# Kernel tuning notes

Measured on AMD Instinct MI355X. Metric: run time of the kernel, lower is better.

Reference implementation:

```python
import jax, jax.numpy as jnp
import numpy as np

SELECT_NUM = 5
N_OBJ = 256


def conv(x, w, b, stride=1, pad=None):
    """NCHW conv. pad=None -> VALID; pad=1 -> [(1,1),(1,1)]."""
    padding = 'VALID' if pad is None else [(pad, pad), (pad, pad)]
    out = jax.lax.conv_general_dilated(
        x, w, (stride, stride), padding,
        dimension_numbers=('NCHW', 'OIHW', 'NCHW'))
    return out + b[None, :, None, None]


def setup_inputs() -> dict:
    key = jax.random.key(0)
    ks = jax.random.split(key, 20)

    def p(k, shape, fan_in):
        return (jax.random.normal(k, shape, jnp.float32) / np.float32(np.sqrt(fan_in)))

    inp = {}
    inp['glob_feature'] = jax.random.normal(ks[0], (1, 1024, 28, 28), jnp.float32)
    inp['roi_features'] = jax.random.normal(ks[1], (N_OBJ, 2048, 7, 7), jnp.float32)
    # valid boxes in a 1280x720 image: x1>x0, y1>y0 so log(.) is finite
    x0 = jax.random.uniform(ks[2], (N_OBJ,), minval=0.0, maxval=600.0)
    y0 = jax.random.uniform(ks[3], (N_OBJ,), minval=0.0, maxval=340.0)
    x1 = x0 + jax.random.uniform(ks[4], (N_OBJ,), minval=10.0, maxval=600.0)
    y1 = y0 + jax.random.uniform(ks[5], (N_OBJ,), minval=10.0, maxval=340.0)
    inp['bbox'] = jnp.stack([x0, y0, x1, y1], axis=1)

    # global branch
    inp['w_glob1'] = p(ks[6], (512, 1024, 4, 4), 1024 * 16); inp['b_glob1'] = jnp.zeros(512, jnp.float32)
    inp['w_glob2'] = p(ks[7], (256, 512, 4, 4), 512 * 16);   inp['b_glob2'] = jnp.zeros(256, jnp.float32)
    # object branch
    inp['w_obj1'] = p(ks[8], (1024, 2048, 3, 3), 2048 * 9);  inp['b_obj1'] = jnp.zeros(1024, jnp.float32)
    inp['w_obj2'] = p(ks[9], (256, 1024, 3, 3), 1024 * 9);   inp['b_obj2'] = jnp.zeros(256, jnp.float32)
    # selector (516 = 260 obj + 256 glob)
    inp['w_sel1'] = p(ks[10], (256, 516, 3, 3), 516 * 9);    inp['b_sel1'] = jnp.zeros(256, jnp.float32)
    inp['w_sel2'] = p(ks[11], (16, 256, 3, 3), 256 * 9);     inp['b_sel2'] = jnp.zeros(16, jnp.float32)
    inp['w_sel3'] = p(ks[12], (1, 16, 3, 3), 16 * 9);        inp['b_sel3'] = jnp.zeros(1, jnp.float32)
    # FC head (eval mode: dropout = identity)
    inp['w_fc1'] = p(ks[13], (516, 256), 516);               inp['b_fc1'] = jnp.zeros(256, jnp.float32)
    inp['w_fc2'] = p(ks[14], (256 * SELECT_NUM, 64), 1280);  inp['b_fc2'] = jnp.zeros(64, jnp.float32)
    inp['w_fc3'] = p(ks[15], (64, 4), 64);                   inp['b_fc3'] = jnp.zeros(4, jnp.float32)
    return inp


def reference(glob_feature, roi_features, bbox,
              w_glob1, b_glob1, w_glob2, b_glob2,
              w_obj1, b_obj1, w_obj2, b_obj2,
              w_sel1, b_sel1, w_sel2, b_sel2, w_sel3, b_sel3,
              w_fc1, b_fc1, w_fc2, b_fc2, w_fc3, b_fc3):
    # global branch: [1,1024,28,28] -> [1,512,14,14] -> [1,256,7,7]; pool(7) is identity
    glob = jax.nn.relu(conv(glob_feature, w_glob1, b_glob1, stride=2, pad=1))
    glob = jax.nn.relu(conv(glob, w_glob2, b_glob2, stride=2, pad=1))

    # object branch: [N,2048,7,7] -> [N,1024,7,7] -> [N,256,7,7]
    obj = jax.nn.relu(conv(roi_features, w_obj1, b_obj1, pad=1))
    obj = jax.nn.relu(conv(obj, w_obj2, b_obj2, pad=1))

    # bbox normalization (uses original coords; image is 1280x720)
    x0, y0, x1, y1 = bbox[:, 0], bbox[:, 1], bbox[:, 2], bbox[:, 3]
    bb = jnp.stack([x0 / 1280.0, y0 / 720.0,
                    jnp.log(1280.0 / (x1 - x0)),
                    jnp.log(720.0 / (y1 - y0))], axis=1)  # [N,4]
    bb = jnp.broadcast_to(bb[:, :, None, None], (bb.shape[0], 4, 7, 7))
    obj = jnp.concatenate([bb, obj], axis=1)  # [N,260,7,7]

    # selector: concat with broadcast glob, 3 valid convs 7->5->3->1
    glob2 = jnp.broadcast_to(glob, (obj.shape[0], 256, 7, 7))
    s = jnp.concatenate([obj, glob2], axis=1)  # [N,516,7,7]
    s = jax.nn.relu(conv(s, w_sel1, b_sel1))
    s = jax.nn.relu(conv(s, w_sel2, b_sel2))
    s = conv(s, w_sel3, b_sel3).reshape(-1)  # [N]

    # top-k selection (sort descending over objects)
    idx = jnp.argsort(-s)[:SELECT_NUM]
    obj = obj[idx] / np.float32(SELECT_NUM)  # [5,260,7,7]

    # adaptive avg pool to 1x1 == mean over HW
    obj = obj.mean(axis=(2, 3))                               # [5,260]
    g = jnp.broadcast_to(glob.mean(axis=(2, 3)), (SELECT_NUM, 256))  # [5,256]
    x = jnp.concatenate([obj, g], axis=1)                     # [5,516]

    x = jax.nn.relu(x @ w_fc1 + b_fc1)   # dropout is identity in eval
    tmp = x.reshape(-1)                  # [1280]
    x = jax.nn.relu(tmp @ w_fc2 + b_fc2) # [64]
    x = x @ w_fc3 + b_fc3                # [4]
    return x
```

## Files before the change

### kernel.cpp

```cpp
#include <hip/hip_runtime.h>
#include <math.h>

using half8 = __attribute__((ext_vector_type(8))) _Float16;
using half4 = __attribute__((ext_vector_type(4))) _Float16;
using f32x4 = __attribute__((ext_vector_type(4))) float;

template<int CIN, int KC, int M_, int BM>
__device__ void transform_w_dev(float* lds, const float* __restrict__ w,
                                _Float16* __restrict__ wt, int s, int m0, int tid) {
  constexpr int NT = (KC / 32) * 9;
  const int ci0 = s * 32;
  int vlen = (CIN - ci0) * 9;
  if (vlen > 288) vlen = 288;
  if (vlen < 0) vlen = 0;
  for (int e = tid; e < 32 * 288; e += 256) {
    const int mi = e / 288, o = e - mi * 288;
    float v = 0.f;
    if (o < vlen) v = w[(size_t)(m0 + mi) * (CIN * 9) + (size_t)ci0 * 9 + o];
    lds[mi * 289 + o] = v;
  }
  __syncthreads();
  const int cc = s >> 2, sub = s & 3;
  int ns = (KC - 128 * cc) / 32; if (ns > 4) ns = 4;
  const int mt = m0 / BM;
  const int mb = m0 - mt * BM;
  _Float16* base = wt + (size_t)mt * NT * (BM * 32);
  for (int u = tid; u < 36 * 256; u += 256) {
    const int chunk = u >> 8, within = u & 255;
    const int g = chunk & 3, khkw = chunk >> 2;
    const int mi = within >> 3, i = within & 7;
    const int kt = 36 * cc + khkw * ns + sub;
    const float v = lds[mi * 289 + (8 * g + i) * 9 + khkw];
    base[(size_t)kt * (BM * 32) + g * (BM * 8) + (mb + mi) * 8 + i] = (_Float16)v;
  }
}

__device__ void convert_tr_dev(_Float16 (*t_s)[136], const float* __restrict__ x,
                               _Float16* __restrict__ xh, int cb, int obj, int tid) {
  const int cbase = cb * 128;
  const float* src = x + (size_t)obj * 2048 * 49 + (size_t)cbase * 49;
  for (int e = tid; e < 128 * 49; e += 256) {
    const int ci = e / 49, pos = e - ci * 49;
    t_s[pos][ci] = (_Float16)src[e];
  }
  __syncthreads();
  _Float16* dst = xh + (size_t)obj * 49 * 2048 + cbase;
  for (int u = tid; u < 49 * 16; u += 256) {
    const int pos = u >> 4, l = u & 15;
    *(half8*)&dst[(size_t)pos * 2048 + l * 8] = *(const half8*)&t_s[pos][l * 8];
  }
}

template<int M_, int CIN, int KH, int KW, int H, int W, int OH, int OW,
         int STRIDE, int PAD, int BATCH, int OUTC, int CO_OFF, bool RELU,
         int TM, int TN, int KSPLIT, bool PARTIAL>
__device__ void conv_gemm_dev(char* shraw, const float* __restrict__ A,
                              const float* __restrict__ X,
                              const float* __restrict__ bias,
                              float* __restrict__ out,
                              int n0, int m0, int kz, int t) {
  constexpr int K   = CIN * KH * KW;
  constexpr int N   = BATCH * OH * OW;
  constexpr int BK  = 16;
  constexpr int BM  = 16 * TM;
  constexpr int BN  = 16 * TN;
  constexpr int KCH = K / KSPLIT;

  float (*a_s)[BM] = (float (*)[BM])shraw;
  float (*b_s)[BN] = (float (*)[BN])(shraw + sizeof(float) * BK * BM);

  const int tx = t & 15;
  const int ty = t >> 4;
  constexpr int AQ    = TM / 4;
  constexpr int TPR_A = 4 / AQ;
  const int am = t / TPR_A;
  const int ak = (t % TPR_A) * (4 * AQ);
  constexpr int BQ = TN / 4;
  const int bk = t & 15;
  const int bn = (t >> 4) * TN;

  float acc[TM][TN];
#pragma unroll
  for (int i = 0; i < TM; i++)
#pragma unroll
    for (int j = 0; j < TN; j++) acc[i][j] = 0.f;

  for (int k0 = kz * KCH; k0 < (kz + 1) * KCH; k0 += BK) {
    float4 av[AQ];
#pragma unroll
    for (int q = 0; q < AQ; q++) {
      av[q] = make_float4(0.f, 0.f, 0.f, 0.f);
      const int kq = k0 + ak + 4 * q;
      if ((m0 + am) < M_ && kq < K)
        av[q] = *reinterpret_cast<const float4*>(&A[(m0 + am) * K + kq]);
    }
    float bv[TN];
#pragma unroll
    for (int q = 0; q < TN; q++) bv[q] = 0.f;
    {
      const int kk = k0 + bk;
      if (kk < K) {
        const int ci = kk / (KH * KW);
        const int r  = kk - ci * (KH * KW);
        const int kh = r / KW;
        const int kw = r - kh * KW;
#pragma unroll
        for (int q = 0; q < TN; q++) {
          const int n = n0 + bn + q;
          if (n < N) {
            const int b   = n / (OH * OW);
            const int pos = n - b * (OH * OW);
            const int oh  = pos / OW;
            const int ow  = pos - oh * OW;
            const int ih  = oh * STRIDE - PAD + kh;
            const int iw  = ow * STRIDE - PAD + kw;
            if (ih >= 0 && ih < H && iw >= 0 && iw < W)
              bv[q] = X[((b * CIN + ci) * H + ih) * W + iw];
          }
        }
      }
    }
    __syncthreads();
#pragma unroll
    for (int q = 0; q < AQ; q++) {
      const int kq = ak + 4 * q;
      a_s[kq + 0][am] = av[q].x;
      a_s[kq + 1][am] = av[q].y;
      a_s[kq + 2][am] = av[q].z;
      a_s[kq + 3][am] = av[q].w;
    }
#pragma unroll
    for (int q = 0; q < BQ; q++)
      *reinterpret_cast<float4*>(&b_s[bk][bn + 4 * q]) =
          make_float4(bv[4 * q], bv[4 * q + 1], bv[4 * q + 2], bv[4 * q + 3]);
    __syncthreads();
#pragma unroll
    for (int kk2 = 0; kk2 < BK; kk2++) {
      float a[TM], b[TN];
#pragma unroll
      for (int q = 0; q < AQ; q++)
        *reinterpret_cast<float4*>(&a[4 * q]) =
            *reinterpret_cast<const float4*>(&a_s[kk2][ty * TM + 4 * q]);
#pragma unroll
      for (int q = 0; q < BQ; q++)
        *reinterpret_cast<float4*>(&b[4 * q]) =
            *reinterpret_cast<const float4*>(&b_s[kk2][tx * TN + 4 * q]);
#pragma unroll
      for (int i = 0; i < TM; i++)
#pragma unroll
        for (int j = 0; j < TN; j++)
          acc[i][j] = fmaf(a[i], b[j], acc[i][j]);
    }
  }

#pragma unroll
  for (int i = 0; i < TM; i++) {
    const int m = m0 + ty * TM + i;
    if (m < M_) {
#pragma unroll
      for (int j = 0; j < TN; j++) {
        const int n = n0 + tx * TN + j;
        if (n < N) {
          if (PARTIAL) {
            out[((size_t)kz * M_ + m) * N + n] = acc[i][j];
          } else {
            float v = acc[i][j] + bias[m];
            if (RELU) v = fmaxf(v, 0.f);
            const int b   = n / (OH * OW);
            const int pos = n - b * (OH * OW);
            out[(b * OUTC + CO_OFF + m) * (OH * OW) + pos] = v;
          }
        }
      }
    }
  }
}

template<int M_, int CIN, int KH, int KW, int H, int W, int OH, int OW,
         int STRIDE, int PAD, int BATCH, int OUTC, int CO_OFF, bool RELU,
         int TM, int TN, int KSPLIT, bool PARTIAL>
__global__ __launch_bounds__(256)
void conv_gemm(const float* __restrict__ A, const float* __restrict__ X,
               const float* __restrict__ bias, float* __restrict__ out) {
  __shared__ char sh[16 * (16 * TM + 16 * TN) * 4];
  conv_gemm_dev<M_, CIN, KH, KW, H, W, OH, OW, STRIDE, PAD, BATCH, OUTC, CO_OFF,
                RELU, TM, TN, KSPLIT, PARTIAL>(
      sh, A, X, bias, out, blockIdx.x * 16 * TN, blockIdx.y * 16 * TM,
      blockIdx.z, threadIdx.x);
}

__global__ __launch_bounds__(256)
void prep1(const float* __restrict__ w_obj1, _Float16* __restrict__ wbuf1,
           const float* __restrict__ roi, _Float16* __restrict__ xh1) {
  __shared__ char sh[32 * 289 * 4];
  int b = blockIdx.x;
  if (b < 2048) {
    transform_w_dev<2048, 2048, 1024, 512>((float*)sh, w_obj1, wbuf1,
                                           b & 63, (b >> 6) * 32, threadIdx.x);
  } else {
    b -= 2048;
    convert_tr_dev((_Float16(*)[136])sh, roi, xh1, b & 15, b >> 4, threadIdx.x);
  }
}

__global__ __launch_bounds__(256)
void prep2(const float* __restrict__ w_obj2, _Float16* __restrict__ wbuf2,
           const float* __restrict__ w_sel1, _Float16* __restrict__ wbufs1,
           const float* __restrict__ w_glob1, const float* __restrict__ gfeat,
           float* __restrict__ part1) {
  __shared__ char sh[32 * 289 * 4];
  int b = blockIdx.x;
  if (b < 256) {
    transform_w_dev<1024, 1024, 256, 128>((float*)sh, w_obj2, wbuf2,
                                          b & 31, (b >> 5) * 32, threadIdx.x);
  } else if (b < 392) {
    b -= 256;
    transform_w_dev<516, 544, 256, 128>((float*)sh, w_sel1, wbufs1,
                                        b % 17, (b / 17) * 32, threadIdx.x);
  } else {
    b -= 392;
    conv_gemm_dev<512, 1024, 4, 4, 28, 28, 14, 14, 2, 1, 1, 512, 0, true,
                  4, 4, 16, true>(sh, w_glob1, gfeat, nullptr, part1,
                                  (b & 3) * 64, ((b >> 2) & 7) * 64, b >> 5,
                                  threadIdx.x);
  }
}

template<int KC, int BM, int FN, int OHW, int PAD, int NMT, int NOP>
__global__ __launch_bounds__(512)
void conv_mfma2(const _Float16* __restrict__ Wt, const _Float16* __restrict__ X,
                const float* __restrict__ bias, _Float16* __restrict__ out,
                int outc, int co_off) {
  constexpr int NT   = (KC / 32) * 9;
  constexpr int OPOS = OHW * OHW;
  constexpr int WM   = BM / 8;
  constexpr int FR   = WM / 16;
  constexpr int NCH  = KC / 128;

  __shared__ alignas(16) _Float16 x_s[2][50][136];

  const int tid  = threadIdx.x;
  const int wid  = tid >> 6;
  const int lane = tid & 63;
  const int g    = lane >> 4;
  const int ln   = lane & 15;
  const int wm   = wid * WM;

  const int bid = blockIdx.x;
  const int j = bid & 7, q = bid >> 3;
  constexpr int OPJ = 8 / NMT;
  const int mt = j / OPJ;
  const int op = (j % OPJ) * (NOP / OPJ) + q;

  if (tid < 272) x_s[tid / 136][49][tid % 136] = (_Float16)0.f;

  int ohv[FN], owv[FN], objv[FN];
  bool pvv[FN];
#pragma unroll
  for (int f = 0; f < FN; f++) {
    const int p = ln + 16 * f;
    pvv[f] = p < 2 * OPOS;
    const int ob = pvv[f] ? (p / OPOS) : 1;
    objv[f] = ob;
    const int pp = pvv[f] ? (p - ob * OPOS) : 0;
    ohv[f] = pp / OHW;
    owv[f] = pp % OHW;
  }

  f32x4 acc[FR][FN];
#pragma unroll
  for (int r = 0; r < FR; r++)
#pragma unroll
    for (int f = 0; f < FN; f++) acc[r][f] = (f32x4){0.f, 0.f, 0.f, 0.f};

  const _Float16* Xh = X + (size_t)(2 * op) * 49 * KC;

  half8 rg[4];
  auto load_chunk = [&](int cbase) {
#pragma unroll
    for (int v = 0; v < 4; v++) {
      const int u = v * 512 + tid;
      if (u < 1568) {
        const int row = u >> 4, l = u & 15;
        const int o = row >= 49 ? 1 : 0, pos = row - 49 * o;
        rg[v] = *(const half8*)(Xh + (size_t)(o * 49 + pos) * KC + cbase + l * 8);
      }
    }
  };
  auto write_chunk = [&]() {
#pragma unroll
    for (int v = 0; v < 4; v++) {
      const int u = v * 512 + tid;
      if (u < 1568) {
        const int row = u >> 4, l = u & 15;
        const int o = row >= 49 ? 1 : 0, pos = row - 49 * o;
        *(half8*)&x_s[o][pos][l * 8] = rg[v];
      }
    }
  };

  const _Float16* ap = Wt + (size_t)mt * NT * (BM * 32) + (g * BM + wm + ln) * 8;
  half8 afA[FR], afB[FR], afC[FR];
#pragma unroll
  for (int r = 0; r < FR; r++) afA[r] = *(const half8*)(ap + r * 128);
  ap += BM * 32;
#pragma unroll
  for (int r = 0; r < FR; r++) afB[r] = *(const half8*)(ap + r * 128);
  ap += BM * 32;

  load_chunk(0);

  auto kstep = [&](half8 (&cur)[FR], half8 (&fut)[FR], int subbyte,
                   const int (&boff)[FN]) {
#pragma unroll
    for (int r = 0; r < FR; r++) fut[r] = *(const half8*)(ap + r * 128);
    ap += BM * 32;
    __builtin_amdgcn_s_setprio(1);
    const char* xb = (const char*)(&x_s[0][0][0]) + subbyte;
#pragma unroll
    for (int f = 0; f < FN; f++) {
      const half8 bf = *(const half8*)(xb + boff[f]);
#pragma unroll
      for (int r = 0; r < FR; r++)
        acc[r][f] = __builtin_amdgcn_mfma_f32_16x16x32_f16(cur[r], bf, acc[r][f], 0, 0, 0);
    }
    __builtin_amdgcn_s_setprio(0);
  };

  for (int c = 0; c < NCH; c++) {
    asm volatile("s_barrier" ::: "memory");
    write_chunk();
    if (c + 1 < NCH) load_chunk((c + 1) * 128);
    asm volatile("s_waitcnt lgkmcnt(0)\n\ts_barrier" ::: "memory");
#pragma unroll
    for (int t9 = 0; t9 < 9; t9++) {
      const int kh = t9 / 3, kw = t9 - 3 * (t9 / 3);
      int boff[FN];
#pragma unroll
      for (int f = 0; f < FN; f++) {
        const int ih = ohv[f] + kh - PAD;
        const int iw = owv[f] + kw - PAD;
        bool v = pvv[f];
        if (PAD) v = v && ((unsigned)ih < 7u) && ((unsigned)iw < 7u);
        const int row = v ? (ih * 7 + iw) : 49;
        boff[f] = (objv[f] * 50 * 136 + row * 136) * 2;
      }
#pragma unroll
      for (int s4 = 0; s4 < 4; s4++) {
        const int ph = (t9 * 4 + s4) % 3;
        const int subbyte = (s4 * 32 + 8 * g) * 2;
        if (ph == 0)      kstep(afA, afC, subbyte, boff);
        else if (ph == 1) kstep(afB, afA, subbyte, boff);
        else              kstep(afC, afB, subbyte, boff);
      }
    }
  }

  _Float16 (*ot_s)[49][132] = (_Float16 (*)[49][132]) & x_s[0][0][0];
  constexpr int PASSES = BM / 128;
#pragma unroll
  for (int p = 0; p < PASSES; p++) {
    asm volatile("s_waitcnt lgkmcnt(0)\n\ts_barrier" ::: "memory");
    if (wm >= 128 * p && wm < 128 * (p + 1)) {
#pragma unroll
      for (int f = 0; f < FN; f++) {
        if (pvv[f]) {
          const int pos = ohv[f] * OHW + owv[f];
          const int ob  = objv[f];
#pragma unroll
          for (int r = 0; r < FR; r++) {
            const int cl = wm - 128 * p + r * 16 + g * 4;
            half4 h;
#pragma unroll
            for (int e = 0; e < 4; e++)
              h[e] = (_Float16)fmaxf(
                  acc[r][f][e] + bias[mt * BM + wm + r * 16 + g * 4 + e], 0.f);
            *(half4*)&ot_s[ob][pos][cl] = h;
          }
        }
      }
    }
    asm volatile("s_waitcnt lgkmcnt(0)\n\ts_barrier" ::: "memory");
    for (int u = tid; u < 2 * OPOS * 32; u += 512) {
      const int row = u >> 5, l = u & 31;
      const int o = row >= OPOS ? 1 : 0, pos = row - OPOS * o;
      const half4 v = *(const half4*)&ot_s[o][pos][l * 4];
      *(half4*)&out[((size_t)(2 * op + o) * OPOS + pos) * outc + co_off +
                    mt * BM + 128 * p + l * 4] = v;
    }
  }
}

template<int KC, int BM, int FN, int OHW, int PAD, bool TOUT, typename OUT_T,
         int NMT, int NOP>
__global__ __launch_bounds__(512)
void conv_mfma(const _Float16* __restrict__ Wt, const _Float16* __restrict__ X,
               const float* __restrict__ bias, OUT_T* __restrict__ out,
               int outc, int co_off) {
  constexpr int NT    = (KC / 32) * 9;
  constexpr int OPOS  = OHW * OHW;
  constexpr int WM    = BM / 4;
  constexpr int FR    = WM / 16;
  constexpr int CFULL = KC / 128;
  constexpr int TAIL  = KC - CFULL * 128;
  constexpr int NCH   = CFULL + (TAIL ? 1 : 0);

  __shared__ alignas(16) _Float16 x_s[2][50][136];

  const int tid  = threadIdx.x;
  const int wid  = tid >> 6;
  const int lane = tid & 63;
  const int g    = lane >> 4;
  const int ln   = lane & 15;
  const int obj  = wid >> 2;
  const int wm   = (wid & 3) * WM;

  const int bid = blockIdx.x;
  const int j = bid & 7, q = bid >> 3;
  constexpr int OPJ = 8 / NMT;
  const int mt = j / OPJ;
  const int op = (j % OPJ) * (NOP / OPJ) + q;

  if (tid < 272) x_s[tid / 136][49][tid % 136] = (_Float16)0.f;

  int ohv[FN], owv[FN];
  bool pvv[FN];
#pragma unroll
  for (int f = 0; f < FN; f++) {
    const int pos = ln + 16 * f;
    pvv[f] = pos < OPOS;
    ohv[f] = pos / OHW;
    owv[f] = pos % OHW;
  }

  f32x4 acc[FR][FN];
#pragma unroll
  for (int r = 0; r < FR; r++)
#pragma unroll
    for (int f = 0; f < FN; f++) acc[r][f] = (f32x4){0.f, 0.f, 0.f, 0.f};

  const _Float16* Xh = X + (size_t)(2 * op) * 49 * KC;

  half8 rg[4];
  auto load_chunk = [&](int cbase, int cw) {
    if (cw == 128) {
#pragma unroll
      for (int v = 0; v < 4; v++) {
        const int u = v * 512 + tid;
        if (u < 1568) {
          const int row = u >> 4, l = u & 15;
          const int o = row >= 49 ? 1 : 0, pos = row - 49 * o;
          rg[v] = *(const half8*)(Xh + (size_t)(o * 49 + pos) * KC + cbase + l * 8);
        }
      }
    } else {
      if (tid < 392) {
        const int row = tid >> 2, l = tid & 3;
        const int o = row >= 49 ? 1 : 0, pos = row - 49 * o;
        rg[0] = *(const half8*)(Xh + (size_t)(o * 49 + pos) * KC + cbase + l * 8);
      }
    }
  };
  auto write_chunk = [&](int cw) {
    if (cw == 128) {
#pragma unroll
      for (int v = 0; v < 4; v++) {
        const int u = v * 512 + tid;
        if (u < 1568) {
          const int row = u >> 4, l = u & 15;
          const int o = row >= 49 ? 1 : 0, pos = row - 49 * o;
          *(half8*)&x_s[o][pos][l * 8] = rg[v];
        }
      }
    } else {
      if (tid < 392) {
        const int row = tid >> 2, l = tid & 3;
        const int o = row >= 49 ? 1 : 0, pos = row - 49 * o;
        *(half8*)&x_s[o][pos][l * 8] = rg[0];
      }
    }
  };

  const _Float16* ap = Wt + (size_t)mt * NT * (BM * 32) + (g * BM + wm + ln) * 8;
  half8 afA[FR], afB[FR], afC[FR];
#pragma unroll
  for (int r = 0; r < FR; r++) afA[r] = *(const half8*)(ap + r * 128);
  ap += BM * 32;
#pragma unroll
  for (int r = 0; r < FR; r++) afB[r] = *(const half8*)(ap + r * 128);
  ap += BM * 32;

  load_chunk(0, KC < 128 ? KC : 128);

  auto kstep = [&](half8 (&cur)[FR], half8 (&fut)[FR], int subbyte,
                   const int (&boff)[FN]) {
#pragma unroll
    for (int r = 0; r < FR; r++) fut[r] = *(const half8*)(ap + r * 128);
    ap += BM * 32;
    __builtin_amdgcn_s_setprio(1);
    const char* xb = (const char*)(&x_s[0][0][0]) + subbyte;
#pragma unroll
    for (int f = 0; f < FN; f++) {
      const half8 bf = *(const half8*)(xb + boff[f]);
#pragma unroll
      for (int r = 0; r < FR; r++)
        acc[r][f] = __builtin_amdgcn_mfma_f32_16x16x32_f16(cur[r], bf, acc[r][f], 0, 0, 0);
    }
    __builtin_amdgcn_s_setprio(0);
  };

  int ktile = 0;
  for (int c = 0; c < NCH; c++) {
    const int cw = (c < CFULL) ? 128 : TAIL;
    asm volatile("s_barrier" ::: "memory");
    write_chunk(cw);
    if (c + 1 < NCH)
      load_chunk((c + 1) * 128, (c + 1 < CFULL) ? 128 : TAIL);
    asm volatile("s_waitcnt lgkmcnt(0)\n\ts_barrier" ::: "memory");
    const int nsub = cw / 32;
    for (int khkw = 0; khkw < 9; khkw++) {
      const int kh = khkw / 3, kw = khkw - 3 * (khkw / 3);
      int boff[FN];
#pragma unroll
      for (int f = 0; f < FN; f++) {
        const int ih = ohv[f] + kh - PAD;
        const int iw = owv[f] + kw - PAD;
        bool v = pvv[f];
        if (PAD) v = v && ((unsigned)ih < 7u) && ((unsigned)iw < 7u);
        const int row = v ? (ih * 7 + iw) : 49;
        boff[f] = (obj * 50 * 136 + row * 136) * 2;
      }
      for (int sub = 0; sub < nsub; sub++) {
        const int ph = ktile % 3;
        const int subbyte = (sub * 32 + 8 * g) * 2;
        if (ph == 0)      kstep(afA, afC, subbyte, boff);
        else if (ph == 1) kstep(afB, afA, subbyte, boff);
        else              kstep(afC, afB, subbyte, boff);
        ktile++;
      }
    }
  }

  if constexpr (TOUT) {
    _Float16 (*ot_s)[49][132] = (_Float16 (*)[49][132]) & x_s[0][0][0];
    asm volatile("s_waitcnt lgkmcnt(0)\n\ts_barrier" ::: "memory");
#pragma unroll
    for (int f = 0; f < FN; f++) {
      const int pos = ln + 16 * f;
      if (pos < OPOS) {
#pragma unroll
        for (int r = 0; r < FR; r++) {
          const int cl = wm + r * 16 + g * 4;
          half4 h;
#pragma unroll
          for (int e = 0; e < 4; e++)
            h[e] = (_Float16)fmaxf(
                acc[r][f][e] + bias[mt * BM + wm + r * 16 + g * 4 + e], 0.f);
          *(half4*)&ot_s[obj][pos][cl] = h;
        }
      }
    }
    asm volatile("s_waitcnt lgkmcnt(0)\n\ts_barrier" ::: "memory");
    _Float16* dst = (_Float16*)out;
    for (int u = tid; u < 2 * OPOS * 32; u += 512) {
      const int row = u >> 5, l = u & 31;
      const int o = row >= OPOS ? 1 : 0, pos = row - OPOS * o;
      const half4 v = *(const half4*)&ot_s[o][pos][l * 4];
      *(half4*)&dst[((size_t)(2 * op + o) * OPOS + pos) * outc + co_off +
                    mt * BM + l * 4] = v;
    }
  } else {
    const int bo = 2 * op + obj;
#pragma unroll
    for (int f = 0; f < FN; f++) {
      const int pos = ln + 16 * f;
      if (pos < OPOS) {
#pragma unroll
        for (int r = 0; r < FR; r++) {
          const int mrow = mt * BM + wm + r * 16 + g * 4;
#pragma unroll
          for (int e = 0; e < 4; e++) {
            const int m = mrow + e;
            float v = fmaxf(acc[r][f][e] + bias[m], 0.f);
            out[((size_t)bo * outc + co_off + m) * OPOS + pos] = (OUT_T)v;
          }
        }
      }
    }
  }
}

__global__ void reduce_bias_relu(const float* __restrict__ part,
                                 const float* __restrict__ bias,
                                 float* __restrict__ out, int MN, int N, int KS) {
  const int e = blockIdx.x * 256 + threadIdx.x;
  if (e >= MN) return;
  float s = 0.f;
  for (int k = 0; k < KS; k++) s += part[(size_t)k * MN + e];
  s += bias[e / N];
  out[e] = fmaxf(s, 0.f);
}

__global__ __launch_bounds__(256)
void sel2_kernel(const float* __restrict__ x, const float* __restrict__ w,
                 const float* __restrict__ b, float* __restrict__ out) {
  const int wv   = (blockIdx.x * 256 + threadIdx.x) >> 6;
  const int lane = threadIdx.x & 63;
  const int obj  = wv >> 4, co = wv & 15;
  float acc[9];
#pragma unroll
  for (int p = 0; p < 9; p++) acc[p] = 0.f;
  const float* xo = x + (size_t)obj * 256 * 25;
  const float* wo = w + (size_t)co * 2304;
  for (int k = lane; k < 2304; k += 64) {
    const int ci = k / 9, rr = k - 9 * ci;
    const int kh = rr / 3, kw = rr - 3 * kh;
    const float wval = wo[k];
    const float* xc = xo + ci * 25;
#pragma unroll
    for (int oh = 0; oh < 3; oh++)
#pragma unroll
      for (int ow = 0; ow < 3; ow++)
        acc[oh * 3 + ow] = fmaf(xc[(oh + kh) * 5 + (ow + kw)], wval, acc[oh * 3 + ow]);
  }
  const float bv = b[co];
#pragma unroll
  for (int p = 0; p < 9; p++) {
    float v = acc[p];
#pragma unroll
    for (int off = 32; off; off >>= 1) v += __shfl_xor(v, off);
    if (lane == 0) out[(size_t)wv * 9 + p] = fmaxf(v + bv, 0.f);
  }
}

__global__ void prep_sin_t(const float* __restrict__ bbox,
                           const float* __restrict__ glob,
                           _Float16* __restrict__ sint) {
  const int b = blockIdx.x;
  const float x0 = bbox[b * 4 + 0], y0 = bbox[b * 4 + 1];
  const float x1 = bbox[b * 4 + 2], y1 = bbox[b * 4 + 3];
  const float bbv[4] = {x0 / 1280.f, y0 / 720.f,
                        logf(1280.f / (x1 - x0)), logf(720.f / (y1 - y0))};
  _Float16* base = sint + (size_t)b * 49 * 544;
  for (int e = threadIdx.x; e < 49 * 288; e += blockDim.x) {
    const int pos = e / 288, q = e - pos * 288;
    float v; int c;
    if (q < 4)        { v = bbv[q];                   c = q; }
    else if (q < 260) { v = glob[(q - 4) * 49 + pos]; c = q + 256; }
    else              { v = 0.f;                      c = q + 256; }
    base[pos * 544 + c] = (_Float16)v;
  }
}

__global__ __launch_bounds__(512)
void head_kernel(const float* __restrict__ sel2, const float* __restrict__ w3,
                 const float* __restrict__ b3, const _Float16* __restrict__ sint,
                 const float* __restrict__ glob, const float* __restrict__ w1,
                 const float* __restrict__ b1, const float* __restrict__ w2,
                 const float* __restrict__ b2, const float* __restrict__ wf3,
                 const float* __restrict__ bf3, float* __restrict__ out) {
  __shared__ float w3_s[144];
  __shared__ float s_s[256];
  __shared__ int   idx_s[5];
  __shared__ float objsel_s[5 * 260];
  __shared__ float g_s[256];
  __shared__ float x1_s[1280];
  __shared__ float x2_s[64];
  const int t = threadIdx.x;
  if (t < 144) w3_s[t] = w3[t];
  __syncthreads();
  if (t < 256) {
    float acc = b3[0];
    const float* p = sel2 + t * 144;
    for (int k = 0; k < 144; k++) acc += p[k] * w3_s[k];
    s_s[t] = acc;
  } else {
    const int c = t - 256;
    float s = 0.f;
    const float* p = glob + c * 49;
    for (int q = 0; q < 49; q++) s += p[q];
    g_s[c] = s * (1.f / 49.f);
  }
  __syncthreads();
  if (t == 0) {
    for (int i = 0; i < 5; i++) {
      float best = -1e30f; int bi = 0;
      for (int j = 0; j < 256; j++)
        if (s_s[j] > best) { best = s_s[j]; bi = j; }
      idx_s[i] = bi;
      s_s[bi] = -1e30f;
    }
  }
  __syncthreads();
  for (int e = t; e < 5 * 260; e += 512) {
    const int i = e / 260, c = e - 260 * i;
    const _Float16* base = sint + (size_t)idx_s[i] * 49 * 544;
    float s = 0.f;
    for (int p = 0; p < 49; p++) s += (float)base[p * 544 + c];
    objsel_s[e] = s * (1.f / 245.f);
  }
  __syncthreads();
  if (t < 256) {
    float acc[5];
#pragma unroll
    for (int i = 0; i < 5; i++) acc[i] = b1[t];
    for (int k = 0; k < 260; k++) {
      const float wv = w1[k * 256 + t];
#pragma unroll
      for (int i = 0; i < 5; i++) acc[i] = fmaf(objsel_s[i * 260 + k], wv, acc[i]);
    }
    for (int k = 260; k < 516; k++) {
      const float wv = w1[k * 256 + t];
      const float gv = g_s[k - 260];
#pragma unroll
      for (int i = 0; i < 5; i++) acc[i] = fmaf(gv, wv, acc[i]);
    }
#pragma unroll
    for (int i = 0; i < 5; i++) x1_s[i * 256 + t] = fmaxf(acc[i], 0.f);
  }
  __syncthreads();
  if (t < 64) {
    float a = b2[t];
    for (int k = 0; k < 1280; k++) a = fmaf(x1_s[k], w2[k * 64 + t], a);
    x2_s[t] = fmaxf(a, 0.f);
  }
  __syncthreads();
  if (t < 4) {
    float a = bf3[t];
    for (int k = 0; k < 64; k++) a = fmaf(x2_s[k], wf3[k * 4 + t], a);
    out[t] = a;
  }
}

extern "C" void kernel_launch(void* const* d_in, const int* in_sizes, int n_in,
                              void* d_out, int out_size, void* d_ws, size_t ws_size,
                              hipStream_t stream) {
  (void)in_sizes; (void)n_in; (void)out_size; (void)ws_size;
  const float* glob_feature = (const float*)d_in[0];
  const float* roi          = (const float*)d_in[1];
  const float* bbox         = (const float*)d_in[2];
  const float* w_glob1      = (const float*)d_in[3];
  const float* b_glob1      = (const float*)d_in[4];
  const float* w_glob2      = (const float*)d_in[5];
  const float* b_glob2      = (const float*)d_in[6];
  const float* w_obj1       = (const float*)d_in[7];
  const float* b_obj1       = (const float*)d_in[8];
  const float* w_obj2       = (const float*)d_in[9];
  const float* b_obj2       = (const float*)d_in[10];
  const float* w_sel1       = (const float*)d_in[11];
  const float* b_sel1       = (const float*)d_in[12];
  const float* w_sel2       = (const float*)d_in[13];
  const float* b_sel2       = (const float*)d_in[14];
  const float* w_sel3       = (const float*)d_in[15];
  const float* b_sel3       = (const float*)d_in[16];
  const float* w_fc1        = (const float*)d_in[17];
  const float* b_fc1        = (const float*)d_in[18];
  const float* w_fc2        = (const float*)d_in[19];
  const float* b_fc2        = (const float*)d_in[20];
  const float* w_fc3        = (const float*)d_in[21];
  const float* b_fc3        = (const float*)d_in[22];

  float* ws = (float*)d_ws;
  _Float16* xh1     = (_Float16*)(ws);
  _Float16* wbuf1   = (_Float16*)(ws + 12845056);
  _Float16* obj1buf = (_Float16*)(ws + 22282240);
  _Float16* sint    = (_Float16*)(ws);
  _Float16* wbuf2   = (_Float16*)(ws + 3411968);
  _Float16* wbufs1  = (_Float16*)(ws + 4591616);
  float*    sel1buf = ws + 5218304;
  float*    glob1buf= ws + 6856704;
  float*    part1   = ws + 6957056;
  float*    part2   = ws + 8562688;
  float*    sel2buf = ws + 8763392;
  float*    globbuf = ws + 8800256;

  prep1<<<dim3(6144), 256, 0, stream>>>(w_obj1, wbuf1, roi, xh1);
  conv_mfma2<2048, 512, 7, 7, 1, 2, 128>
      <<<dim3(256), 512, 0, stream>>>(wbuf1, xh1, b_obj1, obj1buf, 1024, 0);
  prep2<<<dim3(904), 256, 0, stream>>>(w_obj2, wbuf2, w_sel1, wbufs1,
                                       w_glob1, glob_feature, part1);
  reduce_bias_relu<<<dim3(392), 256, 0, stream>>>(part1, b_glob1, glob1buf, 100352, 196, 16);
  conv_gemm<256, 512, 4, 4, 14, 14, 7, 7, 2, 1, 1, 256, 0, true, 4, 4, 16, true>
      <<<dim3(1, 4, 16), 256, 0, stream>>>(w_glob2, glob1buf, b_glob2, part2);
  reduce_bias_relu<<<dim3(49), 256, 0, stream>>>(part2, b_glob2, globbuf, 12544, 49, 16);
  prep_sin_t<<<dim3(256), 256, 0, stream>>>(bbox, globbuf, sint);
  conv_mfma<1024, 128, 4, 7, 1, true, _Float16, 2, 128>
      <<<dim3(256), 512, 0, stream>>>(wbuf2, obj1buf, b_obj2, sint, 544, 4);
  conv_mfma<544, 128, 2, 5, 0, false, float, 2, 128>
      <<<dim3(256), 512, 0, stream>>>(wbufs1, sint, b_sel1, sel1buf, 256, 0);
  sel2_kernel<<<dim3(1024), 256, 0, stream>>>(sel1buf, w_sel2, b_sel2, sel2buf);
  head_kernel<<<dim3(1), 512, 0, stream>>>(sel2buf, w_sel3, b_sel3, sint,
                                           globbuf, w_fc1, b_fc1, w_fc2, b_fc2,
                                           w_fc3, b_fc3, (float*)d_out);
}
```

Measured before the change: 1.008 ms.

## Unify MFMA conv kernels into templated conv_u with smaller 256-thread blocks

Merges the two MFMA implicit-GEMM conv kernels into one template parameterized by wave count and objects per block. The big obj1 conv now uses BM=256 with 4 waves over 512 blocks, and the weight pre-transform tile matches. The obj2 and sel1 convs use one object per block with 4 waves and 512 blocks. The aim is more blocks and better occupancy and CU balance across the 256 CUs. In exchange each block reuses less weight and input data, so more global and LDS traffic is read per FLOP.

```diff
diff --git a/kernel.cpp b/kernel.cpp
--- a/kernel.cpp
+++ b/kernel.cpp
@@ -195,7 +195,7 @@
   __shared__ char sh[32 * 289 * 4];
   int b = blockIdx.x;
   if (b < 2048) {
-    transform_w_dev<2048, 2048, 1024, 512>((float*)sh, w_obj1, wbuf1,
+    transform_w_dev<2048, 2048, 1024, 256>((float*)sh, w_obj1, wbuf1,
                                            b & 63, (b >> 6) * 32, threadIdx.x);
   } else {
     b -= 2048;
@@ -226,18 +226,27 @@
   }
 }
 
-template<int KC, int BM, int FN, int OHW, int PAD, int NMT, int NOP>
-__global__ __launch_bounds__(512)
-void conv_mfma2(const _Float16* __restrict__ Wt, const _Float16* __restrict__ X,
-                const float* __restrict__ bias, _Float16* __restrict__ out,
-                int outc, int co_off) {
-  constexpr int NT   = (KC / 32) * 9;
-  constexpr int OPOS = OHW * OHW;
-  constexpr int WM   = BM / 8;
-  constexpr int FR   = WM / 16;
-  constexpr int NCH  = KC / 128;
-
-  __shared__ alignas(16) _Float16 x_s[2][50][136];
+template<int KC, int BM, int NW, int OBJS, int FN, int OHW, int PAD, bool TOUT,
+         typename OUT_T, int NMT>
+__global__ __launch_bounds__(NW * 64)
+void conv_u(const _Float16* __restrict__ Wt, const _Float16* __restrict__ X,
+            const float* __restrict__ bias, OUT_T* __restrict__ out,
+            int outc, int co_off) {
+  constexpr int NT    = (KC / 32) * 9;
+  constexpr int OPOS  = OHW * OHW;
+  constexpr int WM    = BM / NW;
+  constexpr int FR    = WM / 16;
+  constexpr int NTHR  = NW * 64;
+  constexpr int CFULL = KC / 128;
+  constexpr int TAIL  = KC - CFULL * 128;
+  constexpr int NCH   = CFULL + (TAIL ? 1 : 0);
+  constexpr int NOPB  = 256 / OBJS;
+  constexpr int NU    = OBJS * 49 * 16;
+  constexpr int NV    = (NU + NTHR - 1) / NTHR;
+  constexpr int NUT   = OBJS * 49 * 4;
+  constexpr int NVT   = (NUT + NTHR - 1) / NTHR;
+
+  __shared__ alignas(16) _Float16 x_s[OBJS][50][136];
 
   const int tid  = threadIdx.x;
   const int wid  = tid >> 6;
@@ -249,18 +258,19 @@
   const int bid = blockIdx.x;
   const int j = bid & 7, q = bid >> 3;
   constexpr int OPJ = 8 / NMT;
-  const int mt = j / OPJ;
-  const int op = (j % OPJ) * (NOP / OPJ) + q;
-
-  if (tid < 272) x_s[tid / 136][49][tid % 136] = (_Float16)0.f;
+  const int mt  = j / OPJ;
+  const int opb = (j % OPJ) * (NOPB / OPJ) + q;
+
+  for (int e = tid; e < OBJS * 136; e += NTHR)
+    x_s[e / 136][49][e % 136] = (_Float16)0.f;
 
   int ohv[FN], owv[FN], objv[FN];
   bool pvv[FN];
 #pragma unroll
   for (int f = 0; f < FN; f++) {
     const int p = ln + 16 * f;
-    pvv[f] = p < 2 * OPOS;
-    const int ob = pvv[f] ? (p / OPOS) : 1;
+    pvv[f] = p < OBJS * OPOS;
+    const int ob = pvv[f] ? (p / OPOS) : (OBJS - 1);
     objv[f] = ob;
     const int pp = pvv[f] ? (p - ob * OPOS) : 0;
     ohv[f] = pp / OHW;
@@ -273,28 +283,52 @@
 #pragma unroll
     for (int f = 0; f < FN; f++) acc[r][f] = (f32x4){0.f, 0.f, 0.f, 0.f};
 
-  const _Float16* Xh = X + (size_t)(2 * op) * 49 * KC;
-
-  half8 rg[4];
-  auto load_chunk = [&](int cbase) {
-#pragma unroll
-    for (int v = 0; v < 4; v++) {
-      const int u = v * 512 + tid;
-      if (u < 1568) {
-        const int row = u >> 4, l = u & 15;
-        const int o = row >= 49 ? 1 : 0, pos = row - 49 * o;
-        rg[v] = *(const half8*)(Xh + (size_t)(o * 49 + pos) * KC + cbase + l * 8);
+  const _Float16* Xh = X + (size_t)opb * OBJS * 49 * KC;
+
+  half8 rg[NV];
+  auto load_chunk = [&](int cbase, int cw) {
+    if (cw == 128) {
+#pragma unroll
+      for (int v = 0; v < NV; v++) {
+        const int u = v * NTHR + tid;
+        if (u < NU) {
+          const int row = u >> 4, l = u & 15;
+          const int o = (row >= 49) ? 1 : 0, pos = row - 49 * o;
+          rg[v] = *(const half8*)(Xh + (size_t)(o * 49 + pos) * KC + cbase + l * 8);
+        }
+      }
+    } else {
+#pragma unroll
+      for (int v = 0; v < NVT; v++) {
+        const int u = v * NTHR + tid;
+        if (u < NUT) {
+          const int row = u >> 2, l = u & 3;
+          const int o = (row >= 49) ? 1 : 0, pos = row - 49 * o;
+          rg[v] = *(const half8*)(Xh + (size_t)(o * 49 + pos) * KC + cbase + l * 8);
+        }
       }
     }
   };
-  auto write_chunk = [&]() {
-#pragma unroll
-    for (int v = 0; v < 4; v++) {
-      const int u = v * 512 + tid;
-      if (u < 1568) {
-        const int row = u >> 4, l = u & 15;
-        const int o = row >= 49 ? 1 : 0, pos = row - 49 * o;
-        *(half8*)&x_s[o][pos][l * 8] = rg[v];
+  auto write_chunk = [&](int cw) {
+    if (cw == 128) {
+#pragma unroll
+      for (int v = 0; v < NV; v++) {
+        const int u = v * NTHR + tid;
+        if (u < NU) {
+          const int row = u >> 4, l = u & 15;
+          const int o = (row >= 49) ? 1 : 0, pos = row - 49 * o;
+          *(half8*)&x_s[o][pos][l * 8] = rg[v];
+        }
+      }
+    } else {
+#pragma unroll
+      for (int v = 0; v < NVT; v++) {
+        const int u = v * NTHR + tid;
+        if (u < NUT) {
+          const int row = u >> 2, l = u & 3;
+          const int o = (row >= 49) ? 1 : 0, pos = row - 49 * o;
+          *(half8*)&x_s[o][pos][l * 8] = rg[v];
+        }
       }
     }
   };
@@ -308,7 +342,7 @@
   for (int r = 0; r < FR; r++) afB[r] = *(const half8*)(ap + r * 128);
   ap += BM * 32;
 
-  load_chunk(0);
+  load_chunk(0, KC < 128 ? KC : 128);
 
   auto kstep = [&](half8 (&cur)[FR], half8 (&fut)[FR], int subbyte,
                    const int (&boff)[FN]) {
@@ -328,27 +362,50 @@
   };
 
   for (int c = 0; c < NCH; c++) {
+    const int cw = (c < CFULL) ? 128 : TAIL;
     asm volatile("s_barrier" ::: "memory");
-    write_chunk();
-    if (c + 1 < NCH) load_chunk((c + 1) * 128);
+    write_chunk(cw);
+    if (c + 1 < NCH) load_chunk((c + 1) * 128, (c + 1 < CFULL) ? 128 : TAIL);
     asm volatile("s_waitcnt lgkmcnt(0)\n\ts_barrier" ::: "memory");
-#pragma unroll
-    for (int t9 = 0; t9 < 9; t9++) {
-      const int kh = t9 / 3, kw = t9 - 3 * (t9 / 3);
-      int boff[FN];
-#pragma unroll
-      for (int f = 0; f < FN; f++) {
-        const int ih = ohv[f] + kh - PAD;
-        const int iw = owv[f] + kw - PAD;
-        bool v = pvv[f];
-        if (PAD) v = v && ((unsigned)ih < 7u) && ((unsigned)iw < 7u);
-        const int row = v ? (ih * 7 + iw) : 49;
-        boff[f] = (objv[f] * 50 * 136 + row * 136) * 2;
-      }
-#pragma unroll
-      for (int s4 = 0; s4 < 4; s4++) {
-        const int ph = (t9 * 4 + s4) % 3;
-        const int subbyte = (s4 * 32 + 8 * g) * 2;
+    if (cw == 128) {
+#pragma unroll
+      for (int t9 = 0; t9 < 9; t9++) {
+        const int kh = t9 / 3, kw = t9 - 3 * (t9 / 3);
+        int boff[FN];
+#pragma unroll
+        for (int f = 0; f < FN; f++) {
+          const int ih = ohv[f] + kh - PAD;
+          const int iw = owv[f] + kw - PAD;
+          bool v = pvv[f];
+          if (PAD) v = v && ((unsigned)ih < 7u) && ((unsigned)iw < 7u);
+          const int row = v ? (ih * 7 + iw) : 49;
+          boff[f] = (objv[f] * 50 * 136 + row * 136) * 2;
+        }
+#pragma unroll
+        for (int s4 = 0; s4 < 4; s4++) {
+          const int ph = (t9 * 4 + s4) % 3;
+          const int subbyte = (s4 * 32 + 8 * g) * 2;
+          if (ph == 0)      kstep(afA, afC, subbyte, boff);
+          else if (ph == 1) kstep(afB, afA, subbyte, boff);
+          else              kstep(afC, afB, subbyte, boff);
+        }
+      }
+    } else {
+#pragma unroll
+      for (int t9 = 0; t9 < 9; t9++) {
+        const int kh = t9 / 3, kw = t9 - 3 * (t9 / 3);
+        int boff[FN];
+#pragma unroll
+        for (int f = 0; f < FN; f++) {
+          const int ih = ohv[f] + kh - PAD;
+          const int iw = owv[f] + kw - PAD;
+          bool v = pvv[f];
+          if (PAD) v = v && ((unsigned)ih < 7u) && ((unsigned)iw < 7u);
+          const int row = v ? (ih * 7 + iw) : 49;
+          boff[f] = (objv[f] * 50 * 136 + row * 136) * 2;
+        }
+        const int ph = t9 % 3;
+        const int subbyte = (8 * g) * 2;
         if (ph == 0)      kstep(afA, afC, subbyte, boff);
         else if (ph == 1) kstep(afB, afA, subbyte, boff);
         else              kstep(afC, afB, subbyte, boff);
@@ -356,225 +413,46 @@
     }
   }
 
-  _Float16 (*ot_s)[49][132] = (_Float16 (*)[49][132]) & x_s[0][0][0];
-  constexpr int PASSES = BM / 128;
-#pragma unroll
-  for (int p = 0; p < PASSES; p++) {
-    asm volatile("s_waitcnt lgkmcnt(0)\n\ts_barrier" ::: "memory");
-    if (wm >= 128 * p && wm < 128 * (p + 1)) {
-#pragma unroll
-      for (int f = 0; f < FN; f++) {
-        if (pvv[f]) {
-          const int pos = ohv[f] * OHW + owv[f];
-          const int ob  = objv[f];
-#pragma unroll
-          for (int r = 0; r < FR; r++) {
-            const int cl = wm - 128 * p + r * 16 + g * 4;
-            half4 h;
-#pragma unroll
-            for (int e = 0; e < 4; e++)
-              h[e] = (_Float16)fmaxf(
-                  acc[r][f][e] + bias[mt * BM + wm + r * 16 + g * 4 + e], 0.f);
-            *(half4*)&ot_s[ob][pos][cl] = h;
-          }
-        }
-      }
-    }
-    asm volatile("s_waitcnt lgkmcnt(0)\n\ts_barrier" ::: "memory");
-    for (int u = tid; u < 2 * OPOS * 32; u += 512) {
-      const int row = u >> 5, l = u & 31;
-      const int o = row >= OPOS ? 1 : 0, pos = row - OPOS * o;
-      const half4 v = *(const half4*)&ot_s[o][pos][l * 4];
-      *(half4*)&out[((size_t)(2 * op + o) * OPOS + pos) * outc + co_off +
-                    mt * BM + 128 * p + l * 4] = v;
-    }
-  }
-}
-
-template<int KC, int BM, int FN, int OHW, int PAD, bool TOUT, typename OUT_T,
-         int NMT, int NOP>
-__global__ __launch_bounds__(512)
-void conv_mfma(const _Float16* __restrict__ Wt, const _Float16* __restrict__ X,
-               const float* __restrict__ bias, OUT_T* __restrict__ out,
-               int outc, int co_off) {
-  constexpr int NT    = (KC / 32) * 9;
-  constexpr int OPOS  = OHW * OHW;
-  constexpr int WM    = BM / 4;
-  constexpr int FR    = WM / 16;
-  constexpr int CFULL = KC / 128;
-  constexpr int TAIL  = KC - CFULL * 128;
-  constexpr int NCH   = CFULL + (TAIL ? 1 : 0);
-
-  __shared__ alignas(16) _Float16 x_s[2][50][136];
-
-  const int tid  = threadIdx.x;
-  const int wid  = tid >> 6;
-  const int lane = tid & 63;
-  const int g    = lane >> 4;
-  const int ln   = lane & 15;
-  const int obj  = wid >> 2;
-  const int wm   = (wid & 3) * WM;
-
-  const int bid = blockIdx.x;
-  const int j = bid & 7, q = bid >> 3;
-  constexpr int OPJ = 8 / NMT;
-  const int mt = j / OPJ;
-  const int op = (j % OPJ) * (NOP / OPJ) + q;
-
-  if (tid < 272) x_s[tid / 136][49][tid % 136] = (_Float16)0.f;
-
-  int ohv[FN], owv[FN];
-  bool pvv[FN];
-#pragma unroll
-  for (int f = 0; f < FN; f++) {
-    const int pos = ln + 16 * f;
-    pvv[f] = pos < OPOS;
-    ohv[f] = pos / OHW;
-    owv[f] = pos % OHW;
-  }
-
-  f32x4 acc[FR][FN];
-#pragma unroll
-  for (int r = 0; r < FR; r++)
-#pragma unroll
-    for (int f = 0; f < FN; f++) acc[r][f] = (f32x4){0.f, 0.f, 0.f, 0.f};
-
-  const _Float16* Xh = X + (size_t)(2 * op) * 49 * KC;
-
-  half8 rg[4];
-  auto load_chunk = [&](int cbase, int cw) {
-    if (cw == 128) {
-#pragma unroll
-      for (int v = 0; v < 4; v++) {
-        const int u = v * 512 + tid;
-        if (u < 1568) {
-          const int row = u >> 4, l = u & 15;
-          const int o = row >= 49 ? 1 : 0, pos = row - 49 * o;
-          rg[v] = *(const half8*)(Xh + (size_t)(o * 49 + pos) * KC + cbase + l * 8);
-        }
-      }
-    } else {
-      if (tid < 392) {
-        const int row = tid >> 2, l = tid & 3;
-        const int o = row >= 49 ? 1 : 0, pos = row - 49 * o;
-        rg[0] = *(const half8*)(Xh + (size_t)(o * 49 + pos) * KC + cbase + l * 8);
-      }
-    }
-  };
-  auto write_chunk = [&](int cw) {
-    if (cw == 128) {
-#pragma unroll
-      for (int v = 0; v < 4; v++) {
-        const int u = v * 512 + tid;
-        if (u < 1568) {
-          const int row = u >> 4, l = u & 15;
-          const int o = row >= 49 ? 1 : 0, pos = row - 49 * o;
-          *(half8*)&x_s[o][pos][l * 8] = rg[v];
-        }
-      }
-    } else {
-      if (tid < 392) {
-        const int row = tid >> 2, l = tid & 3;
-        const int o = row >= 49 ? 1 : 0, pos = row - 49 * o;
-        *(half8*)&x_s[o][pos][l * 8] = rg[0];
-      }
-    }
-  };
-
-  const _Float16* ap = Wt + (size_t)mt * NT * (BM * 32) + (g * BM + wm + ln) * 8;
-  half8 afA[FR], afB[FR], afC[FR];
-#pragma unroll
-  for (int r = 0; r < FR; r++) afA[r] = *(const half8*)(ap + r * 128);
-  ap += BM * 32;
-#pragma unroll
-  for (int r = 0; r < FR; r++) afB[r] = *(const half8*)(ap + r * 128);
-  ap += BM * 32;
-
-  load_chunk(0, KC < 128 ? KC : 128);
-
-  auto kstep = [&](half8 (&cur)[FR], half8 (&fut)[FR], int subbyte,
-                   const int (&boff)[FN]) {
-#pragma unroll
-    for (int r = 0; r < FR; r++) fut[r] = *(const half8*)(ap + r * 128);
-    ap += BM * 32;
-    __builtin_amdgcn_s_setprio(1);
-    const char* xb = (const char*)(&x_s[0][0][0]) + subbyte;
-#pragma unroll
-    for (int f = 0; f < FN; f++) {
-      const half8 bf = *(const half8*)(xb + boff[f]);
-#pragma unroll
-      for (int r = 0; r < FR; r++)
-        acc[r][f] = __builtin_amdgcn_mfma_f32_16x16x32_f16(cur[r], bf, acc[r][f], 0, 0, 0);
-    }
-    __builtin_amdgcn_s_setprio(0);
-  };
-
-  int ktile = 0;
-  for (int c = 0; c < NCH; c++) {
-    const int cw = (c < CFULL) ? 128 : TAIL;
-    asm volatile("s_barrier" ::: "memory");
-    write_chunk(cw);
-    if (c + 1 < NCH)
-      load_chunk((c + 1) * 128, (c + 1 < CFULL) ? 128 : TAIL);
-    asm volatile("s_waitcnt lgkmcnt(0)\n\ts_barrier" ::: "memory");
-    const int nsub = cw / 32;
-    for (int khkw = 0; khkw < 9; khkw++) {
-      const int kh = khkw / 3, kw = khkw - 3 * (khkw / 3);
-      int boff[FN];
-#pragma unroll
-      for (int f = 0; f < FN; f++) {
-        const int ih = ohv[f] + kh - PAD;
-        const int iw = owv[f] + kw - PAD;
-        bool v = pvv[f];
-        if (PAD) v = v && ((unsigned)ih < 7u) && ((unsigned)iw < 7u);
-        const int row = v ? (ih * 7 + iw) : 49;
-        boff[f] = (obj * 50 * 136 + row * 136) * 2;
-      }
-      for (int sub = 0; sub < nsub; sub++) {
-        const int ph = ktile % 3;
-        const int subbyte = (sub * 32 + 8 * g) * 2;
-        if (ph == 0)      kstep(afA, afC, subbyte, boff);
-        else if (ph == 1) kstep(afB, afA, subbyte, boff);
-        else              kstep(afC, afB, subbyte, boff);
-        ktile++;
-      }
-    }
-  }
-
   if constexpr (TOUT) {
     _Float16 (*ot_s)[49][132] = (_Float16 (*)[49][132]) & x_s[0][0][0];
-    asm volatile("s_waitcnt lgkmcnt(0)\n\ts_barrier" ::: "memory");
+    constexpr int PASSES = BM / 128;
+#pragma unroll
+    for (int p = 0; p < PASSES; p++) {
+      asm volatile("s_waitcnt lgkmcnt(0)\n\ts_barrier" ::: "memory");
+      if (wm >= 128 * p && wm < 128 * (p + 1)) {
+#pragma unroll
+        for (int f = 0; f < FN; f++) {
+          if (pvv[f]) {
+            const int pos = ohv[f] * OHW + owv[f];
+            const int ob  = objv[f];
+#pragma unroll
+            for (int r = 0; r < FR; r++) {
+              const int cl = wm - 128 * p + r * 16 + g * 4;
+              half4 h;
+#pragma unroll
+              for (int e = 0; e < 4; e++)
+                h[e] = (_Float16)fmaxf(
+                    acc[r][f][e] + bias[mt * BM + wm + r * 16 + g * 4 + e], 0.f);
+              *(half4*)&ot_s[ob][pos][cl] = h;
+            }
+          }
+        }
+      }
+      asm volatile("s_waitcnt lgkmcnt(0)\n\ts_barrier" ::: "memory");
+      for (int u = tid; u < OBJS * OPOS * 32; u += NTHR) {
+        const int row = u >> 5, l = u & 31;
+        const int o = (row >= OPOS) ? 1 : 0, pos = row - OPOS * o;
+        const half4 v = *(const half4*)&ot_s[o][pos][l * 4];
+        *(half4*)&((_Float16*)out)[((size_t)(opb * OBJS + o) * OPOS + pos) * outc +
+                                   co_off + mt * BM + 128 * p + l * 4] = v;
+      }
+    }
+  } else {
 #pragma unroll
     for (int f = 0; f < FN; f++) {
-      const int pos = ln + 16 * f;
-      if (pos < OPOS) {
-#pragma unroll
-        for (int r = 0; r < FR; r++) {
-          const int cl = wm + r * 16 + g * 4;
-          half4 h;
-#pragma unroll
-          for (int e = 0; e < 4; e++)
-            h[e] = (_Float16)fmaxf(
-                acc[r][f][e] + bias[mt * BM + wm + r * 16 + g * 4 + e], 0.f);
-          *(half4*)&ot_s[obj][pos][cl] = h;
-        }
-      }
-    }
-    asm volatile("s_waitcnt lgkmcnt(0)\n\ts_barrier" ::: "memory");
-    _Float16* dst = (_Float16*)out;
-    for (int u = tid; u < 2 * OPOS * 32; u += 512) {
-      const int row = u >> 5, l = u & 31;
-      const int o = row >= OPOS ? 1 : 0, pos = row - OPOS * o;
-      const half4 v = *(const half4*)&ot_s[o][pos][l * 4];
-      *(half4*)&dst[((size_t)(2 * op + o) * OPOS + pos) * outc + co_off +
-                    mt * BM + l * 4] = v;
-    }
-  } else {
-    const int bo = 2 * op + obj;
-#pragma unroll
-    for (int f = 0; f < FN; f++) {
-      const int pos = ln + 16 * f;
-      if (pos < OPOS) {
+      if (pvv[f]) {
+        const int pos = ohv[f] * OHW + owv[f];
+        const int bo  = opb * OBJS + objv[f];
 #pragma unroll
         for (int r = 0; r < FR; r++) {
           const int mrow = mt * BM + wm + r * 16 + g * 4;
@@ -775,8 +653,8 @@
   float*    globbuf = ws + 8800256;
 
   prep1<<<dim3(6144), 256, 0, stream>>>(w_obj1, wbuf1, roi, xh1);
-  conv_mfma2<2048, 512, 7, 7, 1, 2, 128>
-      <<<dim3(256), 512, 0, stream>>>(wbuf1, xh1, b_obj1, obj1buf, 1024, 0);
+  conv_u<2048, 256, 4, 2, 7, 7, 1, true, _Float16, 4>
+      <<<dim3(512), 256, 0, stream>>>(wbuf1, xh1, b_obj1, obj1buf, 1024, 0);
   prep2<<<dim3(904), 256, 0, stream>>>(w_obj2, wbuf2, w_sel1, wbufs1,
                                        w_glob1, glob_feature, part1);
   reduce_bias_relu<<<dim3(392), 256, 0, stream>>>(part1, b_glob1, glob1buf, 100352, 196, 16);
@@ -784,10 +662,10 @@
       <<<dim3(1, 4, 16), 256, 0, stream>>>(w_glob2, glob1buf, b_glob2, part2);
   reduce_bias_relu<<<dim3(49), 256, 0, stream>>>(part2, b_glob2, globbuf, 12544, 49, 16);
   prep_sin_t<<<dim3(256), 256, 0, stream>>>(bbox, globbuf, sint);
-  conv_mfma<1024, 128, 4, 7, 1, true, _Float16, 2, 128>
-      <<<dim3(256), 512, 0, stream>>>(wbuf2, obj1buf, b_obj2, sint, 544, 4);
-  conv_mfma<544, 128, 2, 5, 0, false, float, 2, 128>
-      <<<dim3(256), 512, 0, stream>>>(wbufs1, sint, b_sel1, sel1buf, 256, 0);
+  conv_u<1024, 128, 4, 1, 4, 7, 1, true, _Float16, 2>
+      <<<dim3(512), 256, 0, stream>>>(wbuf2, obj1buf, b_obj2, sint, 544, 4);
+  conv_u<544, 128, 4, 1, 2, 5, 0, false, float, 2>
+      <<<dim3(512), 256, 0, stream>>>(wbufs1, sint, b_sel1, sel1buf, 256, 0);
   sel2_kernel<<<dim3(1024), 256, 0, stream>>>(sel1buf, w_sel2, b_sel2, sel2buf);
   head_kernel<<<dim3(1), 512, 0, stream>>>(sel2buf, w_sel3, b_sel3, sint,
                                            globbuf, w_fc1, b_fc1, w_fc2, b_fc2,
```

Measured after the change: 956.7 us. -5.1%, faster.
